# Optimization experiments

Measured on AMD Instinct MI355X. Metric: run time of the kernel, lower is better.

Reference implementation:

```python
import jax, jax.numpy as jnp
import numpy as np

M = 128      # max_child_num
H = 256      # hidden_size
F = 256      # node_feat_size (must equal H per original view logic)
T = 4        # edge_type_num
I = 2        # num_iterations
NSEM = 57    # Tree.num_sem


def setup_inputs() -> dict:
    key = jax.random.key(0)
    ks = jax.random.split(key, 16)
    def lin(k, shape, fan_in):
        return (jax.random.normal(k, shape, jnp.float32) / np.sqrt(fan_in)).astype(jnp.float32)
    return {
        "parent_feature": jax.random.normal(ks[0], (1, F), jnp.float32),
        "W_parent": lin(ks[1], (F, H * M), F),
        "b_parent": jnp.zeros((H * M,), jnp.float32),
        "W_exists": lin(ks[2], (H, 1), H),
        "b_exists": jnp.zeros((1,), jnp.float32),
        "W_edge_latent": lin(ks[3], (2 * H, H), 2 * H),
        "b_edge_latent": jnp.zeros((H,), jnp.float32),
        "W_edge_exists": lin(ks[4], (T, H), H),   # per-type 1-out linear, stacked
        "b_edge_exists": jnp.zeros((T,), jnp.float32),
        "W_op": lin(ks[5], (I, 3 * H + T, H), 3 * H + T),
        "b_op": jnp.zeros((I, H), jnp.float32),
        "W_child": lin(ks[6], (H * (I + 1), H), H * (I + 1)),
        "b_child": jnp.zeros((H,), jnp.float32),
        "W_sem": lin(ks[7], (H, NSEM), H),
        "b_sem": jnp.zeros((NSEM,), jnp.float32),
        "W_child2": lin(ks[8], (H, F), H),
        "b_child2": jnp.zeros((F,), jnp.float32),
    }


def reference(parent_feature, W_parent, b_parent, W_exists, b_exists,
              W_edge_latent, b_edge_latent, W_edge_exists, b_edge_exists,
              W_op, b_op, W_child, b_child, W_sem, b_sem, W_child2, b_child2):
    # parent -> per-child latents [M, H]
    cf = jax.nn.relu(parent_feature @ W_parent + b_parent).reshape(M, H)
    child_exists_logits = cf @ W_exists + b_exists                      # [M, 1]

    # pairwise edge latents [M, M, H]
    pair = jnp.concatenate([
        jnp.broadcast_to(cf[:, None, :], (M, M, H)),
        jnp.broadcast_to(cf[None, :, :], (M, M, H)),
    ], axis=-1)
    el = jax.nn.relu(pair @ W_edge_latent + b_edge_latent)              # [M, M, H]
    ee = jnp.einsum('ijh,th->ijt', el, W_edge_exists) + b_edge_exists   # [M, M, T]

    # dense-mask equivalent of torch.nonzero edge list: an edge exists per
    # (i, j, type) triple where its logit > 0 and both endpoints exist.
    exists = child_exists_logits[:, 0] > 0                              # [M]
    mask = (ee > 0) & exists[:, None, None] & exists[None, :, None]     # [M, M, T]
    maskf = mask.astype(cf.dtype)

    iter_feats = [cf]
    for i in range(I):
        # node_edge_op input is concat([cf_src, cf_dst, edge_latent, onehot(t)*logit]);
        # split the linear into per-block matmuls to avoid a [M,M,T,3H+T] concat.
        W1, W2, W3, W4 = (W_op[i, :H], W_op[i, H:2 * H],
                          W_op[i, 2 * H:3 * H], W_op[i, 3 * H:])        # W4: [T, H]
        pre = ((cf @ W1)[:, None, None, :]
               + (cf @ W2)[None, :, None, :]
               + (el @ W3)[:, :, None, :]
               + ee[:, :, :, None] * W4[None, None, :, :]
               + b_op[i])                                               # [M, M, T, H]
        h = jax.nn.relu(pre) * maskf[..., None]
        # scatter_max over source index i with zero-initialized output:
        # relu output >= 0 and masked-out edges are 0, so plain max matches.
        cf = jnp.max(h, axis=(1, 2))                                    # [M, H]
        iter_feats.append(cf)

    allf = jnp.concatenate(iter_feats, axis=1)                          # [M, H*(I+1)]
    ch = jax.nn.relu(allf @ W_child + b_child)                          # [M, H]
    child_sem_logits = ch @ W_sem + b_sem                               # [M, NSEM]
    child_feats = jax.nn.relu(ch @ W_child2 + b_child2)                 # [M, F]

    return (child_feats[None], child_sem_logits[None],
            child_exists_logits[None], ee[None])
```

## Files before the change

kernel.cpp:

```cpp
#include <hip/hip_runtime.h>
#include <hip/hip_bf16.h>

#define M_ 128
#define H_ 256
#define F_ 256
#define T_ 4
#define NSEM_ 57

typedef __attribute__((ext_vector_type(8))) short bf16x8;
typedef __attribute__((ext_vector_type(4))) float f32x4;

__device__ __forceinline__ float4 ld4(const float* p) { return *reinterpret_cast<const float4*>(p); }
__device__ __forceinline__ void st4(float* p, float4 v) { *reinterpret_cast<float4*>(p) = v; }
__device__ __forceinline__ float4 add4(float4 a, float4 b) { return make_float4(a.x+b.x, a.y+b.y, a.z+b.z, a.w+b.w); }
__device__ __forceinline__ float4 relu4(float4 a) { return make_float4(fmaxf(a.x,0.f), fmaxf(a.y,0.f), fmaxf(a.z,0.f), fmaxf(a.w,0.f)); }
__device__ __forceinline__ float4 fma4(float s, float4 w, float4 c) { return make_float4(fmaf(s,w.x,c.x), fmaf(s,w.y,c.y), fmaf(s,w.z,c.z), fmaf(s,w.w,c.w)); }

__device__ __forceinline__ unsigned short f2bfu(float x) {
  unsigned u = __float_as_uint(x);
  return (unsigned short)((u + 0x7FFFu + ((u >> 16) & 1u)) >> 16);
}
__device__ __forceinline__ unsigned pack2(float lo, float hi) {
  return (unsigned)f2bfu(lo) | ((unsigned)f2bfu(hi) << 16);
}

__global__ void __launch_bounds__(256) k_parent_partial(
    const float* __restrict__ pf, const float* __restrict__ Wp,
    float* __restrict__ part)
{
  const int cb = (blockIdx.x & 31) * 1024 + threadIdx.x * 4;
  const int kc = blockIdx.x >> 5;
  __shared__ float spf[16];
  if (threadIdx.x < 16) spf[threadIdx.x] = pf[kc * 16 + threadIdx.x];
  __syncthreads();
  const float* w = Wp + (size_t)kc * 16 * 32768 + cb;
  float4 acc = make_float4(0.f, 0.f, 0.f, 0.f);
  #pragma unroll
  for (int k = 0; k < 16; ++k)
    acc = fma4(spf[k], ld4(w + (size_t)k * 32768), acc);
  st4(&part[kc * 32768 + cb], acc);
}

__global__ void __launch_bounds__(256) k_stage1(
    const float* __restrict__ part, const float* __restrict__ bp,
    const float* __restrict__ Wel, const float* __restrict__ Wop0,
    const float* __restrict__ Wex, const float* __restrict__ bex,
    float* __restrict__ cf0, float* __restrict__ A, float* __restrict__ B,
    float* __restrict__ a1, float* __restrict__ a2,
    float* __restrict__ out_ex)
{
  const int m = blockIdx.x >> 1, sel = blockIdx.x & 1;
  const int t = threadIdx.x;
  __shared__ float sall[256];
  __shared__ float red[2][4][256];
  __shared__ float redE[4];

  float v = bp[m * 256 + t];
  #pragma unroll
  for (int q = 0; q < 16; ++q) v += part[q * 32768 + m * 256 + t];
  v = fmaxf(v, 0.f);
  sall[t] = v;
  if (sel == 0) {
    cf0[m * 256 + t] = v;
    float p = v * Wex[t];
    #pragma unroll
    for (int off = 32; off > 0; off >>= 1) p += __shfl_xor(p, off);
    if ((t & 63) == 0) redE[t >> 6] = p;
  }
  __syncthreads();

  const float* W0 = Wel  + (sel ? 65536 : 0);
  const float* W1 = Wop0 + (sel ? 65536 : 0);
  const int hq = (t & 63) << 2, kg = t >> 6, k0 = kg * 64;
  float4 acc0 = make_float4(0.f, 0.f, 0.f, 0.f), acc1 = acc0;
  #pragma unroll 4
  for (int k = k0; k < k0 + 64; ++k) {
    const float s = sall[k];
    acc0 = fma4(s, ld4(W0 + k * 256 + hq), acc0);
    acc1 = fma4(s, ld4(W1 + k * 256 + hq), acc1);
  }
  st4(&red[0][kg][hq], acc0);
  st4(&red[1][kg][hq], acc1);
  __syncthreads();
  if (kg < 2) {
    float4 r = add4(add4(ld4(&red[kg][0][hq]), ld4(&red[kg][1][hq])),
                    add4(ld4(&red[kg][2][hq]), ld4(&red[kg][3][hq])));
    float* dst = (kg == 0) ? (sel ? B : A) : (sel ? a2 : a1);
    st4(&dst[m * 256 + hq], r);
  }
  if (sel == 0 && t == 0)
    out_ex[m] = redE[0] + redE[1] + redE[2] + redE[3] + bex[0];
}

__global__ void __launch_bounds__(256) k_cvt_w(
    const float* __restrict__ Wop, unsigned short* __restrict__ W36F)
{
  const int fb = blockIdx.x;
  const int ct = fb >> 3, kc = fb & 7;
  #pragma unroll
  for (int r = 0; r < 2; ++r) {
    const int e = threadIdx.x * 2 + r;
    const int l = e >> 3, q = e & 7;
    const int c = ct * 16 + (l & 15);
    const int k = kc * 32 + (l >> 4) * 8 + q;
    const int it = c >> 8, h = c & 255;
    W36F[fb * 512 + e] = f2bfu(Wop[(size_t)it * 197632 + (512 + k) * 256 + h]);
  }
}

template<int IT>
__global__ void __launch_bounds__(512) k_gemm_epi(
    const float* __restrict__ Arow, const float* __restrict__ Brow,
    const float* __restrict__ bel, const unsigned short* __restrict__ W36F,
    const float* __restrict__ Wee, const float* __restrict__ bee,
    const float* __restrict__ a1, const float* __restrict__ a2,
    const float* __restrict__ Wop_it, const float* __restrict__ bop_it,
    const float* __restrict__ exlog,
    float* __restrict__ ee_g,
    float* __restrict__ part_op)
{
  const int i  = blockIdx.x >> 2;
  const int jq = blockIdx.x & 3;
  const int t  = threadIdx.x;
  const int w  = t >> 6;
  const int l  = t & 63;
  __shared__ char sEL[32 * 512];
  __shared__ float see[32][4];
  __shared__ float sexf[32];

  const bool exi = exlog[i] > 0.f;

  {
    const int row = t >> 4;
    const int sub = t & 15;
    const int kb  = sub * 16;
    const float* Ap  = Arow + i * 256 + kb;
    const float* Bp  = Brow + (jq * 32 + row) * 256 + kb;
    const float* blp = bel + kb;
    float e[16];
    #pragma unroll
    for (int q = 0; q < 16; q += 4) {
      float4 av = ld4(Ap + q), bv = ld4(Bp + q), lv = ld4(blp + q);
      e[q+0] = fmaxf(av.x + bv.x + lv.x, 0.f);
      e[q+1] = fmaxf(av.y + bv.y + lv.y, 0.f);
      e[q+2] = fmaxf(av.z + bv.z + lv.z, 0.f);
      e[q+3] = fmaxf(av.w + bv.w + lv.w, 0.f);
    }
    if (IT == 0) {
      float s[4] = {0.f, 0.f, 0.f, 0.f};
      #pragma unroll
      for (int tt = 0; tt < 4; ++tt) {
        #pragma unroll
        for (int q = 0; q < 16; q += 4) {
          float4 wv = ld4(Wee + tt * 256 + kb + q);
          s[tt] = fmaf(e[q+0], wv.x, s[tt]);
          s[tt] = fmaf(e[q+1], wv.y, s[tt]);
          s[tt] = fmaf(e[q+2], wv.z, s[tt]);
          s[tt] = fmaf(e[q+3], wv.w, s[tt]);
        }
      }
      #pragma unroll
      for (int off = 1; off < 16; off <<= 1) {
        s[0] += __shfl_xor(s[0], off);
        s[1] += __shfl_xor(s[1], off);
        s[2] += __shfl_xor(s[2], off);
        s[3] += __shfl_xor(s[3], off);
      }
      if (sub < 4) {
        const float v = s[sub] + bee[sub];
        see[row][sub] = v;
        ee_g[(i * 128 + jq * 32 + row) * 4 + sub] = v;
      }
    }
    const int swz = (row & 7) << 4;
    uint4 w0, w1;
    w0.x = pack2(e[0], e[1]);  w0.y = pack2(e[2], e[3]);
    w0.z = pack2(e[4], e[5]);  w0.w = pack2(e[6], e[7]);
    w1.x = pack2(e[8], e[9]);  w1.y = pack2(e[10], e[11]);
    w1.z = pack2(e[12], e[13]); w1.w = pack2(e[14], e[15]);
    *reinterpret_cast<uint4*>(sEL + ((row * 512 + kb * 2)      ^ swz)) = w0;
    *reinterpret_cast<uint4*>(sEL + ((row * 512 + kb * 2 + 16) ^ swz)) = w1;
  }
  if (IT == 1) {
    if (t < 128) see[t >> 2][t & 3] = ee_g[(i * 128 + jq * 32 + (t >> 2)) * 4 + (t & 3)];
  }
  if (t < 32) sexf[t] = exlog[jq * 32 + t];
  __syncthreads();

  const int lr = l & 15, lk = l >> 4;
  f32x4 acc[2][2];
  #pragma unroll
  for (int jt = 0; jt < 2; ++jt)
    #pragma unroll
    for (int ct = 0; ct < 2; ++ct)
      acc[jt][ct] = (f32x4){0.f, 0.f, 0.f, 0.f};

  for (int kc = 0; kc < 8; ++kc) {
    const int r0 = lr, r1 = 16 + lr;
    const int kbyte = kc * 64 + lk * 16;
    bf16x8 af0 = *reinterpret_cast<const bf16x8*>(
        sEL + ((r0 * 512 + kbyte) ^ ((r0 & 7) << 4)));
    bf16x8 af1 = *reinterpret_cast<const bf16x8*>(
        sEL + ((r1 * 512 + kbyte) ^ ((r1 & 7) << 4)));
    #pragma unroll
    for (int ct = 0; ct < 2; ++ct) {
      const int fb = (IT * 16 + w * 2 + ct) * 8 + kc;
      bf16x8 bf = *reinterpret_cast<const bf16x8*>(W36F + fb * 512 + l * 8);
      acc[0][ct] = __builtin_amdgcn_mfma_f32_16x16x32_bf16(af0, bf, acc[0][ct], 0, 0, 0);
      acc[1][ct] = __builtin_amdgcn_mfma_f32_16x16x32_bf16(af1, bf, acc[1][ct], 0, 0, 0);
    }
  }

  const int c0 = w * 32 + lr, c1 = c0 + 16;
  const float b10 = a1[i * 256 + c0] + bop_it[c0];
  const float b11 = a1[i * 256 + c1] + bop_it[c1];
  float w40[4], w41[4];
  #pragma unroll
  for (int tt = 0; tt < 4; ++tt) {
    w40[tt] = Wop_it[(768 + tt) * 256 + c0];
    w41[tt] = Wop_it[(768 + tt) * 256 + c1];
  }
  float am0 = 0.f, am1 = 0.f;
  #pragma unroll
  for (int jt = 0; jt < 2; ++jt) {
    #pragma unroll
    for (int q = 0; q < 4; ++q) {
      const int jrow = jt * 16 + lk * 4 + q;
      const int j = jq * 32 + jrow;
      if (exi && (sexf[jrow] > 0.f)) {
        const float e0 = see[jrow][0], e1 = see[jrow][1];
        const float e2 = see[jrow][2], e3 = see[jrow][3];
        const float pb0 = b10 + a2[j * 256 + c0] + acc[jt][0][q];
        const float pb1 = b11 + a2[j * 256 + c1] + acc[jt][1][q];
        if (e0 > 0.f) { am0 = fmaxf(am0, fmaxf(fmaf(e0, w40[0], pb0), 0.f));
                        am1 = fmaxf(am1, fmaxf(fmaf(e0, w41[0], pb1), 0.f)); }
        if (e1 > 0.f) { am0 = fmaxf(am0, fmaxf(fmaf(e1, w40[1], pb0), 0.f));
                        am1 = fmaxf(am1, fmaxf(fmaf(e1, w41[1], pb1), 0.f)); }
        if (e2 > 0.f) { am0 = fmaxf(am0, fmaxf(fmaf(e2, w40[2], pb0), 0.f));
                        am1 = fmaxf(am1, fmaxf(fmaf(e2, w41[2], pb1), 0.f)); }
        if (e3 > 0.f) { am0 = fmaxf(am0, fmaxf(fmaf(e3, w40[3], pb0), 0.f));
                        am1 = fmaxf(am1, fmaxf(fmaf(e3, w41[3], pb1), 0.f)); }
      }
    }
  }
  am0 = fmaxf(am0, __shfl_xor(am0, 16));
  am0 = fmaxf(am0, __shfl_xor(am0, 32));
  am1 = fmaxf(am1, __shfl_xor(am1, 16));
  am1 = fmaxf(am1, __shfl_xor(am1, 32));
  if (lk == 0) {
    part_op[(i * 4 + jq) * 256 + c0] = am0;
    part_op[(i * 4 + jq) * 256 + c1] = am1;
  }
}

__global__ void __launch_bounds__(256) k_a12b(
    const float* __restrict__ part_op, const float* __restrict__ Wop1,
    float* __restrict__ cf1, float* __restrict__ a1, float* __restrict__ a2)
{
  const int m = blockIdx.x >> 1, sel = blockIdx.x & 1;
  const int t = threadIdx.x;
  __shared__ float sall[256];
  __shared__ float red[4][256];
  float v = part_op[(m * 4 + 0) * 256 + t];
  v = fmaxf(v, part_op[(m * 4 + 1) * 256 + t]);
  v = fmaxf(v, part_op[(m * 4 + 2) * 256 + t]);
  v = fmaxf(v, part_op[(m * 4 + 3) * 256 + t]);
  sall[t] = v;
  if (sel == 0) cf1[m * 256 + t] = v;
  __syncthreads();
  const float* W = Wop1 + (sel ? 65536 : 0);
  const int hq = (t & 63) << 2, kg = t >> 6, k0 = kg * 64;
  float4 acc = make_float4(0.f, 0.f, 0.f, 0.f);
  #pragma unroll 4
  for (int k = k0; k < k0 + 64; ++k)
    acc = fma4(sall[k], ld4(W + k * 256 + hq), acc);
  st4(&red[kg][hq], acc);
  __syncthreads();
  if (kg == 0) {
    float4 r = add4(add4(ld4(&red[0][hq]), ld4(&red[1][hq])),
                    add4(ld4(&red[2][hq]), ld4(&red[3][hq])));
    st4(&((sel ? a2 : a1)[m * 256 + hq]), r);
  }
}

__global__ void __launch_bounds__(256) k_final(
    const float* __restrict__ cf0, const float* __restrict__ cf1,
    const float* __restrict__ part_op,
    const float* __restrict__ Wch, const float* __restrict__ bch,
    const float* __restrict__ Wsem, const float* __restrict__ bsem,
    const float* __restrict__ Wch2, const float* __restrict__ bch2,
    float* __restrict__ out_feats, float* __restrict__ out_sem)
{
  const int m  = blockIdx.x;
  const int t  = threadIdx.x;
  const int hq = (t & 63) << 2;
  const int kg = t >> 6;
  __shared__ float sall[768];
  __shared__ float sch[256];
  __shared__ float red[4][256];
  __shared__ float redS[4][64];

  sall[t]       = cf0[m * 256 + t];
  sall[256 + t] = cf1[m * 256 + t];
  {
    float v = part_op[(m * 4 + 0) * 256 + t];
    v = fmaxf(v, part_op[(m * 4 + 1) * 256 + t]);
    v = fmaxf(v, part_op[(m * 4 + 2) * 256 + t]);
    v = fmaxf(v, part_op[(m * 4 + 3) * 256 + t]);
    sall[512 + t] = v;
  }
  __syncthreads();

  {
    float4 acc = make_float4(0.f, 0.f, 0.f, 0.f);
    const int k0 = kg * 192;
    #pragma unroll 8
    for (int k = k0; k < k0 + 192; ++k)
      acc = fma4(sall[k], ld4(Wch + k * 256 + hq), acc);
    st4(&red[kg][hq], acc);
  }
  __syncthreads();
  if (kg == 0) {
    float4 r = add4(add4(ld4(&red[0][hq]), ld4(&red[1][hq])),
                    add4(ld4(&red[2][hq]), ld4(&red[3][hq])));
    r = relu4(add4(r, ld4(bch + hq)));
    st4(&sch[hq], r);
  }
  __syncthreads();

  {
    float4 f = make_float4(0.f, 0.f, 0.f, 0.f);
    const int k0 = kg * 64;
    #pragma unroll 8
    for (int k = k0; k < k0 + 64; ++k)
      f = fma4(sch[k], ld4(Wch2 + k * 256 + hq), f);
    const int s = t & 63;
    float sv = 0.f;
    if (s < 57) {
      #pragma unroll 8
      for (int k = k0; k < k0 + 64; ++k)
        sv = fmaf(sch[k], Wsem[k * 57 + s], sv);
    }
    redS[kg][s] = sv;
    __syncthreads();
    st4(&red[kg][hq], f);
  }
  __syncthreads();
  if (kg == 0) {
    float4 r = add4(add4(ld4(&red[0][hq]), ld4(&red[1][hq])),
                    add4(ld4(&red[2][hq]), ld4(&red[3][hq])));
    r = relu4(add4(r, ld4(bch2 + hq)));
    st4(&out_feats[m * 256 + hq], r);
    const int s = t & 63;
    if (s < 57)
      out_sem[m * 57 + s] = redS[0][s] + redS[1][s] + redS[2][s] + redS[3][s]
                          + bsem[s];
  }
}

extern "C" void kernel_launch(void* const* d_in, const int* in_sizes, int n_in,
                              void* d_out, int out_size, void* d_ws, size_t ws_size,
                              hipStream_t stream)
{
  const float* pf   = (const float*)d_in[0];
  const float* Wp   = (const float*)d_in[1];
  const float* bp   = (const float*)d_in[2];
  const float* Wex  = (const float*)d_in[3];
  const float* bex  = (const float*)d_in[4];
  const float* Wel  = (const float*)d_in[5];
  const float* bel  = (const float*)d_in[6];
  const float* Wee  = (const float*)d_in[7];
  const float* bee  = (const float*)d_in[8];
  const float* Wop  = (const float*)d_in[9];
  const float* bop  = (const float*)d_in[10];
  const float* Wch  = (const float*)d_in[11];
  const float* bch  = (const float*)d_in[12];
  const float* Wsem = (const float*)d_in[13];
  const float* bsem = (const float*)d_in[14];
  const float* Wch2 = (const float*)d_in[15];
  const float* bch2 = (const float*)d_in[16];

  float* out_feats = (float*)d_out;
  float* out_sem   = out_feats + M_ * F_;
  float* out_ex    = out_sem + M_ * NSEM_;
  float* out_ee    = out_ex + M_;

  float* ws = (float*)d_ws;
  float* cf0 = ws;
  float* cf1 = ws + 32768;
  float* Ab  = ws + 65536;
  float* Bb  = ws + 98304;
  float* a1  = ws + 131072;
  float* a2  = ws + 163840;
  float* part    = ws + 196608;
  float* part_op = ws + 196608;
  unsigned short* W36F = (unsigned short*)(ws + 720896);

  const float* Wop0 = Wop;
  const float* Wop1 = Wop + 197632;

  k_parent_partial<<<512, 256, 0, stream>>>(pf, Wp, part);
  k_stage1<<<256, 256, 0, stream>>>(part, bp, Wel, Wop0, Wex, bex,
                                    cf0, Ab, Bb, a1, a2, out_ex);
  k_cvt_w<<<256, 256, 0, stream>>>(Wop, W36F);

  k_gemm_epi<0><<<512, 512, 0, stream>>>(Ab, Bb, bel, W36F, Wee, bee,
                                         a1, a2, Wop0, bop, out_ex,
                                         out_ee, part_op);
  k_a12b<<<256, 256, 0, stream>>>(part_op, Wop1, cf1, a1, a2);
  k_gemm_epi<1><<<512, 512, 0, stream>>>(Ab, Bb, bel, W36F, Wee, bee,
                                         a1, a2, Wop1, bop + 256, out_ex,
                                         out_ee, part_op);
  k_final<<<128, 256, 0, stream>>>(cf0, cf1, part_op, Wch, bch, Wsem, bsem,
                                   Wch2, bch2, out_feats, out_sem);
}
```

Before: 71.12 us.

## Fuse all stages into one cooperative persistent kernel with grid syncs

```diff
diff --git a/kernel.cpp b/kernel.cpp
--- a/kernel.cpp
+++ b/kernel.cpp
@@ -1,5 +1,8 @@
 #include <hip/hip_runtime.h>
 #include <hip/hip_bf16.h>
+#include <hip/hip_cooperative_groups.h>
+
+namespace cg = cooperative_groups;
 
 #define M_ 128
 #define H_ 256
@@ -24,119 +27,38 @@
   return (unsigned)f2bfu(lo) | ((unsigned)f2bfu(hi) << 16);
 }
 
-__global__ void __launch_bounds__(256) k_parent_partial(
-    const float* __restrict__ pf, const float* __restrict__ Wp,
-    float* __restrict__ part)
+struct Params {
+  const float *pf, *Wp, *bp, *Wex, *bex, *Wel, *bel, *Wee, *bee, *Wop, *bop,
+              *Wch, *bch, *Wsem, *bsem, *Wch2, *bch2;
+  float *out_feats, *out_sem, *out_ex, *out_ee;
+  float *cf0, *cf1, *Ab, *Bb, *a1, *a2, *part, *part_op;
+  unsigned short *W36F;
+};
+
+template<int IT>
+__device__ __forceinline__ void gemm_epi_body(
+    const Params& P, char* smem, int vb, int t)
 {
-  const int cb = (blockIdx.x & 31) * 1024 + threadIdx.x * 4;
-  const int kc = blockIdx.x >> 5;
-  __shared__ float spf[16];
-  if (threadIdx.x < 16) spf[threadIdx.x] = pf[kc * 16 + threadIdx.x];
-  __syncthreads();
-  const float* w = Wp + (size_t)kc * 16 * 32768 + cb;
-  float4 acc = make_float4(0.f, 0.f, 0.f, 0.f);
-  #pragma unroll
-  for (int k = 0; k < 16; ++k)
-    acc = fma4(spf[k], ld4(w + (size_t)k * 32768), acc);
-  st4(&part[kc * 32768 + cb], acc);
-}
-
-__global__ void __launch_bounds__(256) k_stage1(
-    const float* __restrict__ part, const float* __restrict__ bp,
-    const float* __restrict__ Wel, const float* __restrict__ Wop0,
-    const float* __restrict__ Wex, const float* __restrict__ bex,
-    float* __restrict__ cf0, float* __restrict__ A, float* __restrict__ B,
-    float* __restrict__ a1, float* __restrict__ a2,
-    float* __restrict__ out_ex)
-{
-  const int m = blockIdx.x >> 1, sel = blockIdx.x & 1;
-  const int t = threadIdx.x;
-  __shared__ float sall[256];
-  __shared__ float red[2][4][256];
-  __shared__ float redE[4];
-
-  float v = bp[m * 256 + t];
-  #pragma unroll
-  for (int q = 0; q < 16; ++q) v += part[q * 32768 + m * 256 + t];
-  v = fmaxf(v, 0.f);
-  sall[t] = v;
-  if (sel == 0) {
-    cf0[m * 256 + t] = v;
-    float p = v * Wex[t];
-    #pragma unroll
-    for (int off = 32; off > 0; off >>= 1) p += __shfl_xor(p, off);
-    if ((t & 63) == 0) redE[t >> 6] = p;
-  }
-  __syncthreads();
-
-  const float* W0 = Wel  + (sel ? 65536 : 0);
-  const float* W1 = Wop0 + (sel ? 65536 : 0);
-  const int hq = (t & 63) << 2, kg = t >> 6, k0 = kg * 64;
-  float4 acc0 = make_float4(0.f, 0.f, 0.f, 0.f), acc1 = acc0;
-  #pragma unroll 4
-  for (int k = k0; k < k0 + 64; ++k) {
-    const float s = sall[k];
-    acc0 = fma4(s, ld4(W0 + k * 256 + hq), acc0);
-    acc1 = fma4(s, ld4(W1 + k * 256 + hq), acc1);
-  }
-  st4(&red[0][kg][hq], acc0);
-  st4(&red[1][kg][hq], acc1);
-  __syncthreads();
-  if (kg < 2) {
-    float4 r = add4(add4(ld4(&red[kg][0][hq]), ld4(&red[kg][1][hq])),
-                    add4(ld4(&red[kg][2][hq]), ld4(&red[kg][3][hq])));
-    float* dst = (kg == 0) ? (sel ? B : A) : (sel ? a2 : a1);
-    st4(&dst[m * 256 + hq], r);
-  }
-  if (sel == 0 && t == 0)
-    out_ex[m] = redE[0] + redE[1] + redE[2] + redE[3] + bex[0];
-}
-
-__global__ void __launch_bounds__(256) k_cvt_w(
-    const float* __restrict__ Wop, unsigned short* __restrict__ W36F)
-{
-  const int fb = blockIdx.x;
-  const int ct = fb >> 3, kc = fb & 7;
-  #pragma unroll
-  for (int r = 0; r < 2; ++r) {
-    const int e = threadIdx.x * 2 + r;
-    const int l = e >> 3, q = e & 7;
-    const int c = ct * 16 + (l & 15);
-    const int k = kc * 32 + (l >> 4) * 8 + q;
-    const int it = c >> 8, h = c & 255;
-    W36F[fb * 512 + e] = f2bfu(Wop[(size_t)it * 197632 + (512 + k) * 256 + h]);
-  }
-}
-
-template<int IT>
-__global__ void __launch_bounds__(512) k_gemm_epi(
-    const float* __restrict__ Arow, const float* __restrict__ Brow,
-    const float* __restrict__ bel, const unsigned short* __restrict__ W36F,
-    const float* __restrict__ Wee, const float* __restrict__ bee,
-    const float* __restrict__ a1, const float* __restrict__ a2,
-    const float* __restrict__ Wop_it, const float* __restrict__ bop_it,
-    const float* __restrict__ exlog,
-    float* __restrict__ ee_g,
-    float* __restrict__ part_op)
-{
-  const int i  = blockIdx.x >> 2;
-  const int jq = blockIdx.x & 3;
-  const int t  = threadIdx.x;
+  char*  sEL  = smem;
+  float (*see)[4] = reinterpret_cast<float(*)[4]>(smem + 16384);
+  float* sexf = reinterpret_cast<float*>(smem + 16896);
+
+  const int i  = vb >> 2;
+  const int jq = vb & 3;
   const int w  = t >> 6;
   const int l  = t & 63;
-  __shared__ char sEL[32 * 512];
-  __shared__ float see[32][4];
-  __shared__ float sexf[32];
-
-  const bool exi = exlog[i] > 0.f;
+  const float* Wop_it = P.Wop + (size_t)IT * 197632;
+  const float* bop_it = P.bop + IT * 256;
+
+  const bool exi = P.out_ex[i] > 0.f;
 
   {
     const int row = t >> 4;
     const int sub = t & 15;
     const int kb  = sub * 16;
-    const float* Ap  = Arow + i * 256 + kb;
-    const float* Bp  = Brow + (jq * 32 + row) * 256 + kb;
-    const float* blp = bel + kb;
+    const float* Ap  = P.Ab + i * 256 + kb;
+    const float* Bp  = P.Bb + (jq * 32 + row) * 256 + kb;
+    const float* blp = P.bel + kb;
     float e[16];
     #pragma unroll
     for (int q = 0; q < 16; q += 4) {
@@ -152,7 +74,7 @@
       for (int tt = 0; tt < 4; ++tt) {
         #pragma unroll
         for (int q = 0; q < 16; q += 4) {
-          float4 wv = ld4(Wee + tt * 256 + kb + q);
+          float4 wv = ld4(P.Wee + tt * 256 + kb + q);
           s[tt] = fmaf(e[q+0], wv.x, s[tt]);
           s[tt] = fmaf(e[q+1], wv.y, s[tt]);
           s[tt] = fmaf(e[q+2], wv.z, s[tt]);
@@ -167,9 +89,9 @@
         s[3] += __shfl_xor(s[3], off);
       }
       if (sub < 4) {
-        const float v = s[sub] + bee[sub];
+        const float v = s[sub] + P.bee[sub];
         see[row][sub] = v;
-        ee_g[(i * 128 + jq * 32 + row) * 4 + sub] = v;
+        P.out_ee[(i * 128 + jq * 32 + row) * 4 + sub] = v;
       }
     }
     const int swz = (row & 7) << 4;
@@ -182,9 +104,10 @@
     *reinterpret_cast<uint4*>(sEL + ((row * 512 + kb * 2 + 16) ^ swz)) = w1;
   }
   if (IT == 1) {
-    if (t < 128) see[t >> 2][t & 3] = ee_g[(i * 128 + jq * 32 + (t >> 2)) * 4 + (t & 3)];
-  }
-  if (t < 32) sexf[t] = exlog[jq * 32 + t];
+    if (t < 128)
+      see[t >> 2][t & 3] = P.out_ee[(i * 128 + jq * 32 + (t >> 2)) * 4 + (t & 3)];
+  }
+  if (t < 32) sexf[t] = P.out_ex[jq * 32 + t];
   __syncthreads();
 
   const int lr = l & 15, lk = l >> 4;
@@ -205,15 +128,15 @@
     #pragma unroll
     for (int ct = 0; ct < 2; ++ct) {
       const int fb = (IT * 16 + w * 2 + ct) * 8 + kc;
-      bf16x8 bf = *reinterpret_cast<const bf16x8*>(W36F + fb * 512 + l * 8);
+      bf16x8 bf = *reinterpret_cast<const bf16x8*>(P.W36F + fb * 512 + l * 8);
       acc[0][ct] = __builtin_amdgcn_mfma_f32_16x16x32_bf16(af0, bf, acc[0][ct], 0, 0, 0);
       acc[1][ct] = __builtin_amdgcn_mfma_f32_16x16x32_bf16(af1, bf, acc[1][ct], 0, 0, 0);
     }
   }
 
   const int c0 = w * 32 + lr, c1 = c0 + 16;
-  const float b10 = a1[i * 256 + c0] + bop_it[c0];
-  const float b11 = a1[i * 256 + c1] + bop_it[c1];
+  const float b10 = P.a1[i * 256 + c0] + bop_it[c0];
+  const float b11 = P.a1[i * 256 + c1] + bop_it[c1];
   float w40[4], w41[4];
   #pragma unroll
   for (int tt = 0; tt < 4; ++tt) {
@@ -230,8 +153,8 @@
       if (exi && (sexf[jrow] > 0.f)) {
         const float e0 = see[jrow][0], e1 = see[jrow][1];
         const float e2 = see[jrow][2], e3 = see[jrow][3];
-        const float pb0 = b10 + a2[j * 256 + c0] + acc[jt][0][q];
-        const float pb1 = b11 + a2[j * 256 + c1] + acc[jt][1][q];
+        const float pb0 = b10 + P.a2[j * 256 + c0] + acc[jt][0][q];
+        const float pb1 = b11 + P.a2[j * 256 + c1] + acc[jt][1][q];
         if (e0 > 0.f) { am0 = fmaxf(am0, fmaxf(fmaf(e0, w40[0], pb0), 0.f));
                         am1 = fmaxf(am1, fmaxf(fmaf(e0, w41[0], pb1), 0.f)); }
         if (e1 > 0.f) { am0 = fmaxf(am0, fmaxf(fmaf(e1, w40[1], pb0), 0.f));
@@ -248,113 +171,186 @@
   am1 = fmaxf(am1, __shfl_xor(am1, 16));
   am1 = fmaxf(am1, __shfl_xor(am1, 32));
   if (lk == 0) {
-    part_op[(i * 4 + jq) * 256 + c0] = am0;
-    part_op[(i * 4 + jq) * 256 + c1] = am1;
-  }
-}
-
-__global__ void __launch_bounds__(256) k_a12b(
-    const float* __restrict__ part_op, const float* __restrict__ Wop1,
-    float* __restrict__ cf1, float* __restrict__ a1, float* __restrict__ a2)
+    P.part_op[(i * 4 + jq) * 256 + c0] = am0;
+    P.part_op[(i * 4 + jq) * 256 + c1] = am1;
+  }
+}
+
+__global__ void __launch_bounds__(512) k_all(Params P)
 {
-  const int m = blockIdx.x >> 1, sel = blockIdx.x & 1;
-  const int t = threadIdx.x;
-  __shared__ float sall[256];
-  __shared__ float red[4][256];
-  float v = part_op[(m * 4 + 0) * 256 + t];
-  v = fmaxf(v, part_op[(m * 4 + 1) * 256 + t]);
-  v = fmaxf(v, part_op[(m * 4 + 2) * 256 + t]);
-  v = fmaxf(v, part_op[(m * 4 + 3) * 256 + t]);
-  sall[t] = v;
-  if (sel == 0) cf1[m * 256 + t] = v;
-  __syncthreads();
-  const float* W = Wop1 + (sel ? 65536 : 0);
-  const int hq = (t & 63) << 2, kg = t >> 6, k0 = kg * 64;
-  float4 acc = make_float4(0.f, 0.f, 0.f, 0.f);
-  #pragma unroll 4
-  for (int k = k0; k < k0 + 64; ++k)
-    acc = fma4(sall[k], ld4(W + k * 256 + hq), acc);
-  st4(&red[kg][hq], acc);
-  __syncthreads();
-  if (kg == 0) {
-    float4 r = add4(add4(ld4(&red[0][hq]), ld4(&red[1][hq])),
-                    add4(ld4(&red[2][hq]), ld4(&red[3][hq])));
-    st4(&((sel ? a2 : a1)[m * 256 + hq]), r);
-  }
-}
-
-__global__ void __launch_bounds__(256) k_final(
-    const float* __restrict__ cf0, const float* __restrict__ cf1,
-    const float* __restrict__ part_op,
-    const float* __restrict__ Wch, const float* __restrict__ bch,
-    const float* __restrict__ Wsem, const float* __restrict__ bsem,
-    const float* __restrict__ Wch2, const float* __restrict__ bch2,
-    float* __restrict__ out_feats, float* __restrict__ out_sem)
-{
-  const int m  = blockIdx.x;
-  const int t  = threadIdx.x;
-  const int hq = (t & 63) << 2;
-  const int kg = t >> 6;
-  __shared__ float sall[768];
-  __shared__ float sch[256];
-  __shared__ float red[4][256];
-  __shared__ float redS[4][64];
-
-  sall[t]       = cf0[m * 256 + t];
-  sall[256 + t] = cf1[m * 256 + t];
+  cg::grid_group grid = cg::this_grid();
+  const int b = blockIdx.x, t = threadIdx.x;
+  __shared__ __align__(16) char smem[34816];
+
   {
-    float v = part_op[(m * 4 + 0) * 256 + t];
-    v = fmaxf(v, part_op[(m * 4 + 1) * 256 + t]);
-    v = fmaxf(v, part_op[(m * 4 + 2) * 256 + t]);
-    v = fmaxf(v, part_op[(m * 4 + 3) * 256 + t]);
-    sall[512 + t] = v;
-  }
-  __syncthreads();
-
-  {
+    float* spf = reinterpret_cast<float*>(smem);
+    const int kc = b >> 4;
+    if (t < 16) spf[t] = P.pf[kc * 16 + t];
+    __syncthreads();
+    const int col = ((b & 15) * 512 + t) * 4;
+    const float* w = P.Wp + (size_t)kc * 16 * 32768 + col;
     float4 acc = make_float4(0.f, 0.f, 0.f, 0.f);
-    const int k0 = kg * 192;
-    #pragma unroll 8
-    for (int k = k0; k < k0 + 192; ++k)
-      acc = fma4(sall[k], ld4(Wch + k * 256 + hq), acc);
-    st4(&red[kg][hq], acc);
-  }
-  __syncthreads();
-  if (kg == 0) {
-    float4 r = add4(add4(ld4(&red[0][hq]), ld4(&red[1][hq])),
-                    add4(ld4(&red[2][hq]), ld4(&red[3][hq])));
-    r = relu4(add4(r, ld4(bch + hq)));
-    st4(&sch[hq], r);
-  }
-  __syncthreads();
-
-  {
-    float4 f = make_float4(0.f, 0.f, 0.f, 0.f);
-    const int k0 = kg * 64;
-    #pragma unroll 8
+    #pragma unroll
+    for (int k = 0; k < 16; ++k)
+      acc = fma4(spf[k], ld4(w + (size_t)k * 32768), acc);
+    st4(&P.part[kc * 32768 + col], acc);
+
+    const int g = b * 512 + t, fb = g >> 9, e = g & 511;
+    const int ct = fb >> 3, kc2 = fb & 7, l = e >> 3, q = e & 7;
+    const int c = ct * 16 + (l & 15);
+    const int k = kc2 * 32 + (l >> 4) * 8 + q;
+    const int it = c >> 8, h = c & 255;
+    P.W36F[fb * 512 + e] = f2bfu(P.Wop[(size_t)it * 197632 + (512 + k) * 256 + h]);
+  }
+  grid.sync();
+
+  if (b < 128) {
+    float* s1_sall = reinterpret_cast<float*>(smem);
+    float (*s1_red)[2][4][256] =
+        reinterpret_cast<float(*)[2][4][256]>(smem + 1024);
+    float* s1_redE = reinterpret_cast<float*>(smem + 33792);
+    const int m = b, sel = t >> 8, tt = t & 255;
+    if (sel == 0) {
+      float v = P.bp[m * 256 + tt];
+      #pragma unroll
+      for (int q = 0; q < 16; ++q) v += P.part[q * 32768 + m * 256 + tt];
+      v = fmaxf(v, 0.f);
+      s1_sall[tt] = v;
+      P.cf0[m * 256 + tt] = v;
+      float p = v * P.Wex[tt];
+      #pragma unroll
+      for (int off = 32; off > 0; off >>= 1) p += __shfl_xor(p, off);
+      if ((tt & 63) == 0) s1_redE[tt >> 6] = p;
+    }
+    __syncthreads();
+    const float* W0 = P.Wel + (sel ? 65536 : 0);
+    const float* W1 = P.Wop + (sel ? 65536 : 0);
+    const int hq = (tt & 63) << 2, kg = tt >> 6, k0 = kg * 64;
+    float4 acc0 = make_float4(0.f, 0.f, 0.f, 0.f), acc1 = acc0;
+    #pragma unroll 4
+    for (int k = k0; k < k0 + 64; ++k) {
+      const float s = s1_sall[k];
+      acc0 = fma4(s, ld4(W0 + k * 256 + hq), acc0);
+      acc1 = fma4(s, ld4(W1 + k * 256 + hq), acc1);
+    }
+    st4(&s1_red[sel][0][kg][hq], acc0);
+    st4(&s1_red[sel][1][kg][hq], acc1);
+    __syncthreads();
+    if (kg < 2) {
+      float4 r = add4(add4(ld4(&s1_red[sel][kg][0][hq]), ld4(&s1_red[sel][kg][1][hq])),
+                      add4(ld4(&s1_red[sel][kg][2][hq]), ld4(&s1_red[sel][kg][3][hq])));
+      float* dst = (kg == 0) ? (sel ? P.Bb : P.Ab) : (sel ? P.a2 : P.a1);
+      st4(&dst[m * 256 + hq], r);
+    }
+    if (t == 0)
+      P.out_ex[m] = s1_redE[0] + s1_redE[1] + s1_redE[2] + s1_redE[3] + P.bex[0];
+  }
+  grid.sync();
+
+  for (int v = 0; v < 2; ++v) {
+    if (v) __syncthreads();
+    gemm_epi_body<0>(P, smem, b * 2 + v, t);
+  }
+  grid.sync();
+
+  if (b < 128) {
+    float* a_sall = reinterpret_cast<float*>(smem);
+    float (*a_red)[4][256] = reinterpret_cast<float(*)[4][256]>(smem + 1024);
+    const int m = b, sel = t >> 8, tt = t & 255;
+    if (sel == 0) {
+      float v = P.part_op[(m * 4 + 0) * 256 + tt];
+      v = fmaxf(v, P.part_op[(m * 4 + 1) * 256 + tt]);
+      v = fmaxf(v, P.part_op[(m * 4 + 2) * 256 + tt]);
+      v = fmaxf(v, P.part_op[(m * 4 + 3) * 256 + tt]);
+      a_sall[tt] = v;
+      P.cf1[m * 256 + tt] = v;
+    }
+    __syncthreads();
+    const float* W = P.Wop + 197632 + (sel ? 65536 : 0);
+    const int hq = (tt & 63) << 2, kg = tt >> 6, k0 = kg * 64;
+    float4 acc = make_float4(0.f, 0.f, 0.f, 0.f);
+    #pragma unroll 4
     for (int k = k0; k < k0 + 64; ++k)
-      f = fma4(sch[k], ld4(Wch2 + k * 256 + hq), f);
-    const int s = t & 63;
-    float sv = 0.f;
-    if (s < 57) {
+      acc = fma4(a_sall[k], ld4(W + k * 256 + hq), acc);
+    st4(&a_red[sel][kg][hq], acc);
+    __syncthreads();
+    if (kg == 0) {
+      float4 r = add4(add4(ld4(&a_red[sel][0][hq]), ld4(&a_red[sel][1][hq])),
+                      add4(ld4(&a_red[sel][2][hq]), ld4(&a_red[sel][3][hq])));
+      st4(&((sel ? P.a2 : P.a1)[m * 256 + hq]), r);
+    }
+  }
+  grid.sync();
+
+  for (int v = 0; v < 2; ++v) {
+    if (v) __syncthreads();
+    gemm_epi_body<1>(P, smem, b * 2 + v, t);
+  }
+  grid.sync();
+
+  if (b < 128) {
+    float* f_sall = reinterpret_cast<float*>(smem);
+    float* f_sch  = reinterpret_cast<float*>(smem + 3072);
+    float (*f_red)[256] = reinterpret_cast<float(*)[256]>(smem + 4096);
+    float (*f_redS)[64] = reinterpret_cast<float(*)[64]>(smem + 12288);
+    const int m = b, kg = t >> 6, hq = (t & 63) << 2;
+    if (t < 256) {
+      f_sall[t]       = P.cf0[m * 256 + t];
+      f_sall[256 + t] = P.cf1[m * 256 + t];
+      float v = P.part_op[(m * 4 + 0) * 256 + t];
+      v = fmaxf(v, P.part_op[(m * 4 + 1) * 256 + t]);
+      v = fmaxf(v, P.part_op[(m * 4 + 2) * 256 + t]);
+      v = fmaxf(v, P.part_op[(m * 4 + 3) * 256 + t]);
+      f_sall[512 + t] = v;
+    }
+    __syncthreads();
+    {
+      float4 acc = make_float4(0.f, 0.f, 0.f, 0.f);
+      const int k0 = kg * 96;
       #pragma unroll 8
-      for (int k = k0; k < k0 + 64; ++k)
-        sv = fmaf(sch[k], Wsem[k * 57 + s], sv);
-    }
-    redS[kg][s] = sv;
-    __syncthreads();
-    st4(&red[kg][hq], f);
-  }
-  __syncthreads();
-  if (kg == 0) {
-    float4 r = add4(add4(ld4(&red[0][hq]), ld4(&red[1][hq])),
-                    add4(ld4(&red[2][hq]), ld4(&red[3][hq])));
-    r = relu4(add4(r, ld4(bch2 + hq)));
-    st4(&out_feats[m * 256 + hq], r);
-    const int s = t & 63;
-    if (s < 57)
-      out_sem[m * 57 + s] = redS[0][s] + redS[1][s] + redS[2][s] + redS[3][s]
-                          + bsem[s];
+      for (int k = k0; k < k0 + 96; ++k)
+        acc = fma4(f_sall[k], ld4(P.Wch + k * 256 + hq), acc);
+      st4(&f_red[kg][hq], acc);
+    }
+    __syncthreads();
+    if (kg == 0) {
+      float4 r = ld4(&f_red[0][hq]);
+      #pragma unroll
+      for (int g2 = 1; g2 < 8; ++g2) r = add4(r, ld4(&f_red[g2][hq]));
+      r = relu4(add4(r, ld4(P.bch + hq)));
+      st4(&f_sch[hq], r);
+    }
+    __syncthreads();
+    {
+      float4 f = make_float4(0.f, 0.f, 0.f, 0.f);
+      const int k0 = kg * 32;
+      #pragma unroll 8
+      for (int k = k0; k < k0 + 32; ++k)
+        f = fma4(f_sch[k], ld4(P.Wch2 + k * 256 + hq), f);
+      const int s = t & 63;
+      float sv = 0.f;
+      if (s < 57) {
+        #pragma unroll 8
+        for (int k = k0; k < k0 + 32; ++k)
+          sv = fmaf(f_sch[k], P.Wsem[k * 57 + s], sv);
+      }
+      f_redS[kg][s] = sv;
+      st4(&f_red[kg][hq], f);
+    }
+    __syncthreads();
+    if (kg == 0) {
+      float4 r = ld4(&f_red[0][hq]);
+      #pragma unroll
+      for (int g2 = 1; g2 < 8; ++g2) r = add4(r, ld4(&f_red[g2][hq]));
+      r = relu4(add4(r, ld4(P.bch2 + hq)));
+      st4(&P.out_feats[m * 256 + hq], r);
+    }
+    if (t < 57) {
+      float s2 = P.bsem[t];
+      #pragma unroll
+      for (int g2 = 0; g2 < 8; ++g2) s2 += f_redS[g2][t];
+      P.out_sem[m * 57 + t] = s2;
+    }
   }
 }
 
@@ -362,55 +358,41 @@
                               void* d_out, int out_size, void* d_ws, size_t ws_size,
                               hipStream_t stream)
 {
-  const float* pf   = (const float*)d_in[0];
-  const float* Wp   = (const float*)d_in[1];
-  const float* bp   = (const float*)d_in[2];
-  const float* Wex  = (const float*)d_in[3];
-  const float* bex  = (const float*)d_in[4];
-  const float* Wel  = (const float*)d_in[5];
-  const float* bel  = (const float*)d_in[6];
-  const float* Wee  = (const float*)d_in[7];
-  const float* bee  = (const float*)d_in[8];
-  const float* Wop  = (const float*)d_in[9];
-  const float* bop  = (const float*)d_in[10];
-  const float* Wch  = (const float*)d_in[11];
-  const float* bch  = (const float*)d_in[12];
-  const float* Wsem = (const float*)d_in[13];
-  const float* bsem = (const float*)d_in[14];
-  const float* Wch2 = (const float*)d_in[15];
-  const float* bch2 = (const float*)d_in[16];
-
-  float* out_feats = (float*)d_out;
-  float* out_sem   = out_feats + M_ * F_;
-  float* out_ex    = out_sem + M_ * NSEM_;
-  float* out_ee    = out_ex + M_;
+  Params P;
+  P.pf   = (const float*)d_in[0];
+  P.Wp   = (const float*)d_in[1];
+  P.bp   = (const float*)d_in[2];
+  P.Wex  = (const float*)d_in[3];
+  P.bex  = (const float*)d_in[4];
+  P.Wel  = (const float*)d_in[5];
+  P.bel  = (const float*)d_in[6];
+  P.Wee  = (const float*)d_in[7];
+  P.bee  = (const float*)d_in[8];
+  P.Wop  = (const float*)d_in[9];
+  P.bop  = (const float*)d_in[10];
+  P.Wch  = (const float*)d_in[11];
+  P.bch  = (const float*)d_in[12];
+  P.Wsem = (const float*)d_in[13];
+  P.bsem = (const float*)d_in[14];
+  P.Wch2 = (const float*)d_in[15];
+  P.bch2 = (const float*)d_in[16];
+
+  P.out_feats = (float*)d_out;
+  P.out_sem   = P.out_feats + M_ * F_;
+  P.out_ex    = P.out_sem + M_ * NSEM_;
+  P.out_ee    = P.out_ex + M_;
 
   float* ws = (float*)d_ws;
-  float* cf0 = ws;
-  float* cf1 = ws + 32768;
-  float* Ab  = ws + 65536;
-  float* Bb  = ws + 98304;
-  float* a1  = ws + 131072;
-  float* a2  = ws + 163840;
-  float* part    = ws + 196608;
-  float* part_op = ws + 196608;
-  unsigned short* W36F = (unsigned short*)(ws + 720896);
-
-  const float* Wop0 = Wop;
-  const float* Wop1 = Wop + 197632;
-
-  k_parent_partial<<<512, 256, 0, stream>>>(pf, Wp, part);
-  k_stage1<<<256, 256, 0, stream>>>(part, bp, Wel, Wop0, Wex, bex,
-                                    cf0, Ab, Bb, a1, a2, out_ex);
-  k_cvt_w<<<256, 256, 0, stream>>>(Wop, W36F);
-
-  k_gemm_epi<0><<<512, 512, 0, stream>>>(Ab, Bb, bel, W36F, Wee, bee,
-                                         a1, a2, Wop0, bop, out_ex,
-                                         out_ee, part_op);
-  k_a12b<<<256, 256, 0, stream>>>(part_op, Wop1, cf1, a1, a2);
-  k_gemm_epi<1><<<512, 512, 0, stream>>>(Ab, Bb, bel, W36F, Wee, bee,
-                                         a1, a2, Wop1, bop + 256, out_ex,
-                                         out_ee, part_op);
-  k_final<<<128, 256, 0, stream>>>(cf0, cf1, part_op, Wch, bch, Wsem, bsem,
-                                   Wch2, bch2, out_feats, out_sem);
-}
+  P.cf0 = ws;
+  P.cf1 = ws + 32768;
+  P.Ab  = ws + 65536;
+  P.Bb  = ws + 98304;
+  P.a1  = ws + 131072;
+  P.a2  = ws + 163840;
+  P.part    = ws + 196608;
+  P.part_op = ws + 196608;
+  P.W36F = (unsigned short*)(ws + 720896);
+
+  void* args[] = { &P };
+  hipLaunchCooperativeKernel(k_all, dim3(256), dim3(512), args, 0, stream);
+}
```

Result: slower. 225.1 us (+216.5%).
